# Performance work log

Measured on AMD Instinct MI355X. Metric: run time of the kernel, lower is better.

Reference implementation:

```python
import jax, jax.numpy as jnp
import numpy as np


def ternarize_weight(w):
    # abs-mean threshold quantization to {-am, 0, +am}
    abs_mean = jnp.maximum(jnp.abs(w).mean(), 1e-5)
    thr = 0.7 * abs_mean
    q = jnp.where(w > thr, 1.0, jnp.where(w < -thr, -1.0, 0.0))
    # STE: forward value is q*abs_mean, grad flows to w as identity
    return w + jax.lax.stop_gradient(q * abs_mean - w)


def rotate_half(x):
    x1, x2 = jnp.split(x, 2, axis=-1)
    return jnp.concatenate([-x2, x1], axis=-1)


def setup_inputs() -> dict:
    key = jax.random.key(0)
    k1, k2, k3, k4, k5 = jax.random.split(key, 5)
    B, T, C, H = 2, 2048, 1024, 16
    D = C // H
    x = jax.random.normal(k1, (B, T, C), dtype=jnp.float32)
    cos = jax.random.uniform(k2, (1, 1, T, D), dtype=jnp.float32)
    sin = jax.random.uniform(k3, (1, 1, T, D), dtype=jnp.float32)
    w_qkv = jax.random.normal(k4, (3 * C, C), dtype=jnp.float32) / np.sqrt(C)
    w_proj = jax.random.normal(k5, (C, C), dtype=jnp.float32) / np.sqrt(C)
    return {"x": x, "cos": cos, "sin": sin, "w_qkv": w_qkv, "w_proj": w_proj}


def reference(x, cos, sin, w_qkv, w_proj):
    B, T, C = x.shape
    H = 16
    D = C // H
    wq = ternarize_weight(w_qkv)
    wp = ternarize_weight(w_proj)
    qkv = x @ wq.T  # [B,T,3C]
    q, k, v = jnp.split(qkv, 3, axis=-1)
    # [B,T,C] -> [B,H,T,D]
    q = q.reshape(B, T, H, D).transpose(0, 2, 1, 3)
    k = k.reshape(B, T, H, D).transpose(0, 2, 1, 3)
    v = v.reshape(B, T, H, D).transpose(0, 2, 1, 3)
    # RoPE
    q = q * cos + rotate_half(q) * sin
    k = k * cos + rotate_half(k) * sin
    # causal SDPA
    scale = 1.0 / np.sqrt(D)
    scores = jnp.einsum("bhqd,bhkd->bhqk", q, k) * scale
    causal = jnp.tril(jnp.ones((T, T), dtype=bool))
    scores = jnp.where(causal, scores, jnp.finfo(scores.dtype).min)
    attn = jax.nn.softmax(scores, axis=-1)
    y = jnp.einsum("bhqk,bhkd->bhqd", attn, v)  # [B,H,T,D]
    y = y.transpose(0, 2, 1, 3).reshape(B, T, C)
    return y @ wp.T
```

## Files before the change

kernel.cpp:

```cpp
#include <hip/hip_runtime.h>
#include <hip/hip_bf16.h>

#define B_ 2
#define T_ 2048
#define C_ 1024
#define H_ 16
#define D_ 64
#define M_ 4096
#define N3C 3072

using short8  = __attribute__((ext_vector_type(8))) short;
using floatx4 = __attribute__((ext_vector_type(4))) float;
typedef unsigned int u32;

__device__ __forceinline__ unsigned short f2b(float f) {
  __hip_bfloat16 h = __float2bfloat16(f);
  return *reinterpret_cast<unsigned short*>(&h);
}
__device__ __forceinline__ float b2f(unsigned short u) {
  union { unsigned int i; float f; } x; x.i = ((unsigned int)u) << 16; return x.f;
}
__device__ __forceinline__ u32 pk2(float a, float b) {
  float2 t; t.x = a; t.y = b;
  __hip_bfloat162 p = __float22bfloat162_rn(t);
  return *reinterpret_cast<u32*>(&p);
}

__device__ __forceinline__ void gll16(const void* g, void* l) {
  __builtin_amdgcn_global_load_lds((const __attribute__((address_space(1))) u32*)g,
                                   (__attribute__((address_space(3))) u32*)l, 16, 0, 0);
}


__global__ void abs_sum2(const float* __restrict__ wq, const float* __restrict__ wp,
                         double* __restrict__ sums) {
  __shared__ double red[4];
  const float* w = blockIdx.y ? wp : wq;
  const int n4 = blockIdx.y ? (C_ * C_ / 4) : (3 * C_ * C_ / 4);
  int stride = gridDim.x * blockDim.x;
  double s = 0.0;
  for (int i = blockIdx.x * blockDim.x + threadIdx.x; i < n4; i += stride) {
    float4 v = ((const float4*)w)[i];
    s += (double)fabsf(v.x) + (double)fabsf(v.y) + (double)fabsf(v.z) + (double)fabsf(v.w);
  }
  #pragma unroll
  for (int off = 32; off > 0; off >>= 1)
    s += __shfl_down(s, off, 64);
  if ((threadIdx.x & 63) == 0) red[threadIdx.x >> 6] = s;
  __syncthreads();
  if (threadIdx.x == 0) atomicAdd(sums + blockIdx.y, (red[0] + red[1]) + (red[2] + red[3]));
}

__global__ void tern_cvt(const float* __restrict__ wq, const float* __restrict__ wp,
                         const float* __restrict__ x,
                         unsigned short* __restrict__ oq, unsigned short* __restrict__ op,
                         unsigned short* __restrict__ xb,
                         const double* __restrict__ sums, float* __restrict__ ams) {
  const int NQ = 3 * C_ * C_;
  const int NP = C_ * C_;
  int i = blockIdx.x * blockDim.x + threadIdx.x;
  float am0 = fmaxf((float)(sums[0] * (1.0 / NQ)), 1e-5f);
  float am1 = fmaxf((float)(sums[1] * (1.0 / NP)), 1e-5f);
  if (i == 0) { ams[0] = am0; ams[1] = am1; }
  if (i < NQ) {
    float thr = 0.7f * am0, v = wq[i];
    oq[i] = (v > thr) ? 0x3F80u : ((v < -thr) ? 0xBF80u : 0u);
  } else if (i < NQ + NP) {
    int j = i - NQ;
    float thr = 0.7f * am1, v = wp[j];
    op[j] = (v > thr) ? 0x3F80u : ((v < -thr) ? 0xBF80u : 0u);
  } else {
    int j = i - NQ - NP;
    float4 v = ((const float4*)x)[j];
    ushort4 o; o.x = f2b(v.x); o.y = f2b(v.y); o.z = f2b(v.z); o.w = f2b(v.w);
    ((ushort4*)xb)[j] = o;
  }
}


__global__ __launch_bounds__(256) void gemm_qkv(const unsigned short* __restrict__ A,
                                                const unsigned short* __restrict__ W,
                                                const float* __restrict__ scale_ptr,
                                                const float* __restrict__ cosp,
                                                const float* __restrict__ sinp,
                                                unsigned short* __restrict__ Qb,
                                                unsigned short* __restrict__ Kb,
                                                unsigned short* __restrict__ Vtb) {
  const int K = C_;
  __shared__ __attribute__((aligned(16))) unsigned short As[128 * 32];
  __shared__ __attribute__((aligned(16))) unsigned short Ws[128 * 32];
  const int tid = threadIdx.x, lane = tid & 63, wv = tid >> 6;
  const int m = lane & 15, g = lane >> 4;
  const int m0 = blockIdx.y * 128, n0 = blockIdx.x * 128;
  const int wm = (wv >> 1) * 64, wn = (wv & 1) * 64;

  const int srow = wv * 16 + (lane >> 2);
  const int skoff = (lane & 3) * 8;
  const unsigned short* ga0 = A + (size_t)(m0 + srow) * K + skoff;
  const unsigned short* ga1 = A + (size_t)(m0 + 64 + srow) * K + skoff;
  const unsigned short* gw0 = W + (size_t)(n0 + srow) * K + skoff;
  const unsigned short* gw1 = W + (size_t)(n0 + 64 + srow) * K + skoff;
  unsigned short* la0 = As + (wv * 16) * 32;
  unsigned short* la1 = As + (64 + wv * 16) * 32;
  unsigned short* lw0 = Ws + (wv * 16) * 32;
  unsigned short* lw1 = Ws + (64 + wv * 16) * 32;

  floatx4 acc[4][4] = {};
  for (int kc = 0; kc < K; kc += 32) {
    __syncthreads();
    gll16(ga0, la0); gll16(ga1, la1); gll16(gw0, lw0); gll16(gw1, lw1);
    ga0 += 32; ga1 += 32; gw0 += 32; gw1 += 32;
    __syncthreads();
    short8 af[4], wf[4];
    #pragma unroll
    for (int r = 0; r < 4; r++)
      af[r] = *(const short8*)&As[(wm + r * 16 + m) * 32 + g * 8];
    #pragma unroll
    for (int c = 0; c < 4; c++)
      wf[c] = *(const short8*)&Ws[(wn + c * 16 + m) * 32 + g * 8];
    #pragma unroll
    for (int r = 0; r < 4; r++)
      #pragma unroll
      for (int c = 0; c < 4; c++)
        acc[r][c] = __builtin_amdgcn_mfma_f32_16x16x32_bf16(af[r], wf[c], acc[r][c], 0, 0, 0);
  }

  const float am = *scale_ptr;
  const int sect = n0 >> 10;
  const int nloc = n0 & 1023;
  const int h = (nloc + wn) >> 6;
  if (sect < 2) {
    unsigned short* dst = sect ? Kb : Qb;
    const float sc = sect ? am : am * 0.18033688011112042f;
    #pragma unroll
    for (int r = 0; r < 4; r++)
      #pragma unroll
      for (int i = 0; i < 4; i++) {
        int row = m0 + wm + r * 16 + g * 4 + i;
        int t = row & (T_ - 1), b = row >> 11;
        size_t obase = ((size_t)(b * H_ + h) * T_ + t) * 64;
        #pragma unroll
        for (int c = 0; c < 4; c++) {
          int p = c * 16 + m;
          float cv = cosp[t * 64 + p], sv = sinp[t * 64 + p];
          float a = acc[r][c][i], pt = acc[r][c ^ 2][i];
          float val = (c < 2) ? (a * cv - pt * sv) : (a * cv + pt * sv);
          dst[obase + p] = f2b(val * sc);
        }
      }
  } else {
    #pragma unroll
    for (int r = 0; r < 4; r++)
      #pragma unroll
      for (int i = 0; i < 4; i++) {
        int row = m0 + wm + r * 16 + g * 4 + i;
        int t = row & (T_ - 1), b = row >> 11;
        size_t hbase = (size_t)(b * H_ + h) * 64 * T_;
        #pragma unroll
        for (int c = 0; c < 4; c++)
          Vtb[hbase + (size_t)(c * 16 + m) * T_ + t] = f2b(acc[r][c][i] * am);
      }
  }
}


__global__ __launch_bounds__(256) void gemm_proj(const unsigned short* __restrict__ A,
                                                 const unsigned short* __restrict__ W,
                                                 const float* __restrict__ scale_ptr,
                                                 float* __restrict__ Cout) {
  const int K = C_, N = C_;
  __shared__ __attribute__((aligned(16))) unsigned short As[128 * 32];
  __shared__ __attribute__((aligned(16))) unsigned short Ws[64 * 32];
  const int tid = threadIdx.x, lane = tid & 63, wv = tid >> 6;
  const int m = lane & 15, g = lane >> 4;
  const int m0 = blockIdx.y * 128, n0 = blockIdx.x * 64;
  const int wm = (wv >> 1) * 64, wn = (wv & 1) * 32;

  const int srow = wv * 16 + (lane >> 2);
  const int skoff = (lane & 3) * 8;
  const unsigned short* ga0 = A + (size_t)(m0 + srow) * K + skoff;
  const unsigned short* ga1 = A + (size_t)(m0 + 64 + srow) * K + skoff;
  const unsigned short* gw0 = W + (size_t)(n0 + srow) * K + skoff;
  unsigned short* la0 = As + (wv * 16) * 32;
  unsigned short* la1 = As + (64 + wv * 16) * 32;
  unsigned short* lw0 = Ws + (wv * 16) * 32;

  floatx4 acc[4][2] = {};
  for (int kc = 0; kc < K; kc += 32) {
    __syncthreads();
    gll16(ga0, la0); gll16(ga1, la1); gll16(gw0, lw0);
    ga0 += 32; ga1 += 32; gw0 += 32;
    __syncthreads();
    short8 af[4], wf[2];
    #pragma unroll
    for (int r = 0; r < 4; r++)
      af[r] = *(const short8*)&As[(wm + r * 16 + m) * 32 + g * 8];
    #pragma unroll
    for (int c = 0; c < 2; c++)
      wf[c] = *(const short8*)&Ws[(wn + c * 16 + m) * 32 + g * 8];
    #pragma unroll
    for (int r = 0; r < 4; r++)
      #pragma unroll
      for (int c = 0; c < 2; c++)
        acc[r][c] = __builtin_amdgcn_mfma_f32_16x16x32_bf16(af[r], wf[c], acc[r][c], 0, 0, 0);
  }

  const float scale = *scale_ptr;
  #pragma unroll
  for (int r = 0; r < 4; r++)
    #pragma unroll
    for (int c = 0; c < 2; c++)
      #pragma unroll
      for (int i = 0; i < 4; i++) {
        int row = m0 + wm + r * 16 + g * 4 + i;
        int col = n0 + wn + c * 16 + m;
        Cout[(size_t)row * N + col] = acc[r][c][i] * scale;
      }
}


__global__ __launch_bounds__(256) void flash_mfma(const unsigned short* __restrict__ Qb,
                                                  const unsigned short* __restrict__ Kb,
                                                  const unsigned short* __restrict__ Vtb,
                                                  unsigned short* __restrict__ Y) {
  __shared__ __align__(16) unsigned short Ktile[2][64][64];
  __shared__ __align__(16) unsigned short Vtile[2][64][64];
  __shared__ __align__(16) unsigned short Plds[4][16][72];
  const int lane = threadIdx.x & 63;
  const int wv = threadIdx.x >> 6;
  const int m = lane & 15, g = lane >> 4;
  const int gid = blockIdx.x;
  const int xcd = gid & 7, j = gid >> 3;
  const int bh = xcd * 4 + (j & 3);
  const int s = 31 - (j >> 2);
  const int b = bh >> 4, h = bh & 15;
  const size_t hb = (size_t)bh * T_ * 64;
  const unsigned short* Kbh = Kb + hb;
  const unsigned short* Vbh = Vtb + hb;
  const int r8 = lane >> 3, cc8 = lane & 7;
  const int gcol = ((cc8 ^ r8) << 3);

  const int ntiles = s + 1;
  const int qbase = s * 64 + wv * 16;
  const int q_glob = qbase + m;

  const unsigned short* qp = Qb + hb + (size_t)(qbase + m) * 64 + g * 8;
  short8 qf0 = *(const short8*)qp;
  short8 qf1 = *(const short8*)(qp + 32);

  short8 ones;
  #pragma unroll
  for (int i = 0; i < 8; i++) ones[i] = (short)0x3F80;

  floatx4 O[4] = {};
  floatx4 accl = {};

  #pragma unroll
  for (int cc = 0; cc < 2; cc++) {
    int row = wv * 16 + cc * 8;
    gll16(Kbh + (size_t)(row + r8) * 64 + gcol, &Ktile[0][row][0]);
    gll16(Vbh + (size_t)(row + r8) * T_ + gcol, &Vtile[0][row][0]);
  }

  for (int kt = 0; kt < ntiles; kt++) {
    const int buf = kt & 1;
    const int kb = kt * 64;
    __syncthreads();
    if (kt + 1 < ntiles) {
      const int kb2 = kb + 64;
      #pragma unroll
      for (int cc = 0; cc < 2; cc++) {
        int row = wv * 16 + cc * 8;
        gll16(Kbh + (size_t)(kb2 + row + r8) * 64 + gcol, &Ktile[1 - buf][row][0]);
        gll16(Vbh + (size_t)(row + r8) * T_ + kb2 + gcol, &Vtile[1 - buf][row][0]);
      }
    }
    floatx4 S[4];
    #pragma unroll
    for (int mt = 0; mt < 4; mt++) {
      int row = mt * 16 + m;
      short8 kf0 = *(const short8*)&Ktile[buf][row][(g ^ (m & 7)) << 3];
      short8 kf1 = *(const short8*)&Ktile[buf][row][((g + 4) ^ (m & 7)) << 3];
      floatx4 sv = {};
      sv = __builtin_amdgcn_mfma_f32_16x16x32_bf16(kf0, qf0, sv, 0, 0, 0);
      sv = __builtin_amdgcn_mfma_f32_16x16x32_bf16(kf1, qf1, sv, 0, 0, 0);
      S[mt] = sv;
    }
    if (kt + 1 < ntiles) {
      #pragma unroll
      for (int mt = 0; mt < 4; mt++) {
        uint2 w;
        w.x = pk2(exp2f(S[mt][0]), exp2f(S[mt][1]));
        w.y = pk2(exp2f(S[mt][2]), exp2f(S[mt][3]));
        *(uint2*)&Plds[wv][m][mt * 16 + g * 4] = w;
      }
    } else {
      #pragma unroll
      for (int mt = 0; mt < 4; mt++) {
        float e[4];
        #pragma unroll
        for (int r = 0; r < 4; r++) {
          int kg = kb + mt * 16 + g * 4 + r;
          e[r] = (kg <= q_glob) ? exp2f(S[mt][r]) : 0.f;
        }
        uint2 w;
        w.x = pk2(e[0], e[1]);
        w.y = pk2(e[2], e[3]);
        *(uint2*)&Plds[wv][m][mt * 16 + g * 4] = w;
      }
    }
    short8 pa0 = *(const short8*)&Plds[wv][m][g * 8];
    short8 pa1 = *(const short8*)&Plds[wv][m][32 + g * 8];
    #pragma unroll
    for (int nt = 0; nt < 4; nt++) {
      int row = nt * 16 + m;
      short8 v0 = *(const short8*)&Vtile[buf][row][(g ^ (m & 7)) << 3];
      short8 v1 = *(const short8*)&Vtile[buf][row][((g + 4) ^ (m & 7)) << 3];
      O[nt] = __builtin_amdgcn_mfma_f32_16x16x32_bf16(pa0, v0, O[nt], 0, 0, 0);
      O[nt] = __builtin_amdgcn_mfma_f32_16x16x32_bf16(pa1, v1, O[nt], 0, 0, 0);
    }
    accl = __builtin_amdgcn_mfma_f32_16x16x32_bf16(pa0, ones, accl, 0, 0, 0);
    accl = __builtin_amdgcn_mfma_f32_16x16x32_bf16(pa1, ones, accl, 0, 0, 0);
  }

  float li[4];
  #pragma unroll
  for (int r = 0; r < 4; r++) li[r] = 1.0f / accl[r];
  #pragma unroll
  for (int nt = 0; nt < 4; nt++)
    #pragma unroll
    for (int r = 0; r < 4; r++) {
      int trow = qbase + g * 4 + r;
      int col = h * 64 + nt * 16 + m;
      Y[(size_t)(b * T_ + trow) * C_ + col] = f2b(O[nt][r] * li[r]);
    }
}


extern "C" void kernel_launch(void* const* d_in, const int* in_sizes, int n_in,
                              void* d_out, int out_size, void* d_ws, size_t ws_size,
                              hipStream_t stream) {
  (void)in_sizes; (void)n_in; (void)out_size; (void)ws_size;
  const float* x      = (const float*)d_in[0];
  const float* cosp   = (const float*)d_in[1];
  const float* sinp   = (const float*)d_in[2];
  const float* w_qkv  = (const float*)d_in[3];
  const float* w_proj = (const float*)d_in[4];
  float* out = (float*)d_out;

  char* ws = (char*)d_ws;
  double* sums = (double*)ws;
  float*  ams  = (float*)(ws + 16);
  unsigned short* wqkv_b  = (unsigned short*)(ws + 256);
  unsigned short* wproj_b = wqkv_b + (size_t)N3C * C_;
  unsigned short* xb      = wproj_b + (size_t)C_ * C_;
  unsigned short* Qb      = xb + (size_t)M_ * C_;
  unsigned short* Kb      = Qb + (size_t)B_ * H_ * T_ * D_;
  unsigned short* Vtb     = Kb + (size_t)B_ * H_ * T_ * D_;
  unsigned short* yb      = Vtb + (size_t)B_ * H_ * T_ * D_;

  hipMemsetAsync(sums, 0, 16, stream);
  abs_sum2<<<dim3(256, 2), 256, 0, stream>>>(w_qkv, w_proj, sums);
  tern_cvt<<<(4 * C_ * C_ + M_ * C_ / 4) / 256, 256, 0, stream>>>(w_qkv, w_proj, x,
                                                                  wqkv_b, wproj_b, xb,
                                                                  sums, ams);
  gemm_qkv<<<dim3(N3C / 128, M_ / 128), 256, 0, stream>>>(xb, wqkv_b, ams + 0,
                                                          cosp, sinp, Qb, Kb, Vtb);
  flash_mfma<<<1024, 256, 0, stream>>>(Qb, Kb, Vtb, yb);
  gemm_proj<<<dim3(C_ / 64, M_ / 128), 256, 0, stream>>>(yb, wproj_b, ams + 1, out);
}
```

Measured before the change: 207.3 us.

## Double-buffer LDS tiles and XOR-swizzle layout in QKV and proj GEMMs

```diff
diff --git a/kernel.cpp b/kernel.cpp
--- a/kernel.cpp
+++ b/kernel.cpp
@@ -87,37 +87,43 @@
                                                 unsigned short* __restrict__ Kb,
                                                 unsigned short* __restrict__ Vtb) {
   const int K = C_;
-  __shared__ __attribute__((aligned(16))) unsigned short As[128 * 32];
-  __shared__ __attribute__((aligned(16))) unsigned short Ws[128 * 32];
+  __shared__ __attribute__((aligned(16))) unsigned short As[2][128 * 32];
+  __shared__ __attribute__((aligned(16))) unsigned short Ws[2][128 * 32];
   const int tid = threadIdx.x, lane = tid & 63, wv = tid >> 6;
   const int m = lane & 15, g = lane >> 4;
   const int m0 = blockIdx.y * 128, n0 = blockIdx.x * 128;
   const int wm = (wv >> 1) * 64, wn = (wv & 1) * 64;
 
   const int srow = wv * 16 + (lane >> 2);
-  const int skoff = (lane & 3) * 8;
+  const int skoff = (((lane & 3) ^ ((lane >> 2) & 3)) * 8);
   const unsigned short* ga0 = A + (size_t)(m0 + srow) * K + skoff;
   const unsigned short* ga1 = A + (size_t)(m0 + 64 + srow) * K + skoff;
   const unsigned short* gw0 = W + (size_t)(n0 + srow) * K + skoff;
   const unsigned short* gw1 = W + (size_t)(n0 + 64 + srow) * K + skoff;
-  unsigned short* la0 = As + (wv * 16) * 32;
-  unsigned short* la1 = As + (64 + wv * 16) * 32;
-  unsigned short* lw0 = Ws + (wv * 16) * 32;
-  unsigned short* lw1 = Ws + (64 + wv * 16) * 32;
+  const int oA0 = (wv * 16) * 32;
+  const int oA1 = (64 + wv * 16) * 32;
 
   floatx4 acc[4][4] = {};
+  gll16(ga0, &As[0][oA0]); gll16(ga1, &As[0][oA1]);
+  gll16(gw0, &Ws[0][oA0]); gll16(gw1, &Ws[0][oA1]);
+  ga0 += 32; ga1 += 32; gw0 += 32; gw1 += 32;
+
+  const int swz = (g ^ (m & 3)) << 3;
   for (int kc = 0; kc < K; kc += 32) {
+    const int buf = (kc >> 5) & 1;
     __syncthreads();
-    gll16(ga0, la0); gll16(ga1, la1); gll16(gw0, lw0); gll16(gw1, lw1);
-    ga0 += 32; ga1 += 32; gw0 += 32; gw1 += 32;
-    __syncthreads();
+    if (kc + 32 < K) {
+      gll16(ga0, &As[buf ^ 1][oA0]); gll16(ga1, &As[buf ^ 1][oA1]);
+      gll16(gw0, &Ws[buf ^ 1][oA0]); gll16(gw1, &Ws[buf ^ 1][oA1]);
+      ga0 += 32; ga1 += 32; gw0 += 32; gw1 += 32;
+    }
     short8 af[4], wf[4];
     #pragma unroll
     for (int r = 0; r < 4; r++)
-      af[r] = *(const short8*)&As[(wm + r * 16 + m) * 32 + g * 8];
+      af[r] = *(const short8*)&As[buf][(wm + r * 16 + m) * 32 + swz];
     #pragma unroll
     for (int c = 0; c < 4; c++)
-      wf[c] = *(const short8*)&Ws[(wn + c * 16 + m) * 32 + g * 8];
+      wf[c] = *(const short8*)&Ws[buf][(wn + c * 16 + m) * 32 + swz];
     #pragma unroll
     for (int r = 0; r < 4; r++)
       #pragma unroll
@@ -169,35 +175,41 @@
                                                  const float* __restrict__ scale_ptr,
                                                  float* __restrict__ Cout) {
   const int K = C_, N = C_;
-  __shared__ __attribute__((aligned(16))) unsigned short As[128 * 32];
-  __shared__ __attribute__((aligned(16))) unsigned short Ws[64 * 32];
+  __shared__ __attribute__((aligned(16))) unsigned short As[2][128 * 32];
+  __shared__ __attribute__((aligned(16))) unsigned short Ws[2][64 * 32];
   const int tid = threadIdx.x, lane = tid & 63, wv = tid >> 6;
   const int m = lane & 15, g = lane >> 4;
   const int m0 = blockIdx.y * 128, n0 = blockIdx.x * 64;
   const int wm = (wv >> 1) * 64, wn = (wv & 1) * 32;
 
   const int srow = wv * 16 + (lane >> 2);
-  const int skoff = (lane & 3) * 8;
+  const int skoff = (((lane & 3) ^ ((lane >> 2) & 3)) * 8);
   const unsigned short* ga0 = A + (size_t)(m0 + srow) * K + skoff;
   const unsigned short* ga1 = A + (size_t)(m0 + 64 + srow) * K + skoff;
   const unsigned short* gw0 = W + (size_t)(n0 + srow) * K + skoff;
-  unsigned short* la0 = As + (wv * 16) * 32;
-  unsigned short* la1 = As + (64 + wv * 16) * 32;
-  unsigned short* lw0 = Ws + (wv * 16) * 32;
+  const int oA0 = (wv * 16) * 32;
+  const int oA1 = (64 + wv * 16) * 32;
 
   floatx4 acc[4][2] = {};
+  gll16(ga0, &As[0][oA0]); gll16(ga1, &As[0][oA1]); gll16(gw0, &Ws[0][oA0]);
+  ga0 += 32; ga1 += 32; gw0 += 32;
+
+  const int swz = (g ^ (m & 3)) << 3;
   for (int kc = 0; kc < K; kc += 32) {
+    const int buf = (kc >> 5) & 1;
     __syncthreads();
-    gll16(ga0, la0); gll16(ga1, la1); gll16(gw0, lw0);
-    ga0 += 32; ga1 += 32; gw0 += 32;
-    __syncthreads();
+    if (kc + 32 < K) {
+      gll16(ga0, &As[buf ^ 1][oA0]); gll16(ga1, &As[buf ^ 1][oA1]);
+      gll16(gw0, &Ws[buf ^ 1][oA0]);
+      ga0 += 32; ga1 += 32; gw0 += 32;
+    }
     short8 af[4], wf[2];
     #pragma unroll
     for (int r = 0; r < 4; r++)
-      af[r] = *(const short8*)&As[(wm + r * 16 + m) * 32 + g * 8];
+      af[r] = *(const short8*)&As[buf][(wm + r * 16 + m) * 32 + swz];
     #pragma unroll
     for (int c = 0; c < 2; c++)
-      wf[c] = *(const short8*)&Ws[(wn + c * 16 + m) * 32 + g * 8];
+      wf[c] = *(const short8*)&Ws[buf][(wn + c * 16 + m) * 32 + swz];
     #pragma unroll
     for (int r = 0; r < 4; r++)
       #pragma unroll
```

New measurement: 213.9 us. 3.2% more time.

## Triple-buffer LDS staging in QKV and projection GEMMs with vmcnt-based sync

Applied to the files above, without the earlier changes.

```diff
diff --git a/kernel.cpp b/kernel.cpp
--- a/kernel.cpp
+++ b/kernel.cpp
@@ -30,6 +30,12 @@
   __builtin_amdgcn_global_load_lds((const __attribute__((address_space(1))) u32*)g,
                                    (__attribute__((address_space(3))) u32*)l, 16, 0, 0);
 }
+
+#define SYNCV(N) do {                                                   \
+    asm volatile("s_waitcnt vmcnt(" #N ")" ::: "memory");               \
+    __builtin_amdgcn_s_barrier();                                       \
+    asm volatile("" ::: "memory");                                      \
+  } while (0)
 
 
 __global__ void abs_sum2(const float* __restrict__ wq, const float* __restrict__ wp,
@@ -87,8 +93,8 @@
                                                 unsigned short* __restrict__ Kb,
                                                 unsigned short* __restrict__ Vtb) {
   const int K = C_;
-  __shared__ __attribute__((aligned(16))) unsigned short As[128 * 32];
-  __shared__ __attribute__((aligned(16))) unsigned short Ws[128 * 32];
+  __shared__ __attribute__((aligned(16))) unsigned short As[3][128 * 32];
+  __shared__ __attribute__((aligned(16))) unsigned short Ws[3][128 * 32];
   const int tid = threadIdx.x, lane = tid & 63, wv = tid >> 6;
   const int m = lane & 15, g = lane >> 4;
   const int m0 = blockIdx.y * 128, n0 = blockIdx.x * 128;
@@ -100,30 +106,44 @@
   const unsigned short* ga1 = A + (size_t)(m0 + 64 + srow) * K + skoff;
   const unsigned short* gw0 = W + (size_t)(n0 + srow) * K + skoff;
   const unsigned short* gw1 = W + (size_t)(n0 + 64 + srow) * K + skoff;
-  unsigned short* la0 = As + (wv * 16) * 32;
-  unsigned short* la1 = As + (64 + wv * 16) * 32;
-  unsigned short* lw0 = Ws + (wv * 16) * 32;
-  unsigned short* lw1 = Ws + (64 + wv * 16) * 32;
+  const int oA0 = (wv * 16) * 32;
+  const int oA1 = (64 + wv * 16) * 32;
 
   floatx4 acc[4][4] = {};
-  for (int kc = 0; kc < K; kc += 32) {
-    __syncthreads();
-    gll16(ga0, la0); gll16(ga1, la1); gll16(gw0, lw0); gll16(gw1, lw1);
-    ga0 += 32; ga1 += 32; gw0 += 32; gw1 += 32;
-    __syncthreads();
-    short8 af[4], wf[4];
-    #pragma unroll
-    for (int r = 0; r < 4; r++)
-      af[r] = *(const short8*)&As[(wm + r * 16 + m) * 32 + g * 8];
-    #pragma unroll
-    for (int c = 0; c < 4; c++)
-      wf[c] = *(const short8*)&Ws[(wn + c * 16 + m) * 32 + g * 8];
-    #pragma unroll
-    for (int r = 0; r < 4; r++)
-      #pragma unroll
-      for (int c = 0; c < 4; c++)
-        acc[r][c] = __builtin_amdgcn_mfma_f32_16x16x32_bf16(af[r], wf[c], acc[r][c], 0, 0, 0);
-  }
+
+#define QSTAGE(TGT) do {                                                  \
+    gll16(ga0, &As[TGT][oA0]); gll16(ga1, &As[TGT][oA1]);                 \
+    gll16(gw0, &Ws[TGT][oA0]); gll16(gw1, &Ws[TGT][oA1]);                 \
+    ga0 += 32; ga1 += 32; gw0 += 32; gw1 += 32;                           \
+  } while (0)
+
+#define QCOMP(CUR) do {                                                   \
+    short8 af[4], wf[4];                                                  \
+    _Pragma("unroll")                                                     \
+    for (int r = 0; r < 4; r++)                                           \
+      af[r] = *(const short8*)&As[CUR][(wm + r * 16 + m) * 32 + g * 8];   \
+    _Pragma("unroll")                                                     \
+    for (int c = 0; c < 4; c++)                                           \
+      wf[c] = *(const short8*)&Ws[CUR][(wn + c * 16 + m) * 32 + g * 8];   \
+    _Pragma("unroll")                                                     \
+    for (int r = 0; r < 4; r++)                                           \
+      _Pragma("unroll")                                                   \
+      for (int c = 0; c < 4; c++)                                         \
+        acc[r][c] = __builtin_amdgcn_mfma_f32_16x16x32_bf16(af[r], wf[c], acc[r][c], 0, 0, 0); \
+  } while (0)
+
+  QSTAGE(0);
+  QSTAGE(1);
+  SYNCV(4);
+  for (int tt = 0; tt < 10; ++tt) {
+    QSTAGE(2); QCOMP(0); SYNCV(4);
+    QSTAGE(0); QCOMP(1); SYNCV(4);
+    QSTAGE(1); QCOMP(2); SYNCV(4);
+  }
+  QCOMP(0); SYNCV(0);
+  QCOMP(1);
+#undef QSTAGE
+#undef QCOMP
 
   const float am = *scale_ptr;
   const int sect = n0 >> 10;
@@ -169,8 +189,8 @@
                                                  const float* __restrict__ scale_ptr,
                                                  float* __restrict__ Cout) {
   const int K = C_, N = C_;
-  __shared__ __attribute__((aligned(16))) unsigned short As[128 * 32];
-  __shared__ __attribute__((aligned(16))) unsigned short Ws[64 * 32];
+  __shared__ __attribute__((aligned(16))) unsigned short As[3][128 * 32];
+  __shared__ __attribute__((aligned(16))) unsigned short Ws[3][64 * 32];
   const int tid = threadIdx.x, lane = tid & 63, wv = tid >> 6;
   const int m = lane & 15, g = lane >> 4;
   const int m0 = blockIdx.y * 128, n0 = blockIdx.x * 64;
@@ -181,29 +201,44 @@
   const unsigned short* ga0 = A + (size_t)(m0 + srow) * K + skoff;
   const unsigned short* ga1 = A + (size_t)(m0 + 64 + srow) * K + skoff;
   const unsigned short* gw0 = W + (size_t)(n0 + srow) * K + skoff;
-  unsigned short* la0 = As + (wv * 16) * 32;
-  unsigned short* la1 = As + (64 + wv * 16) * 32;
-  unsigned short* lw0 = Ws + (wv * 16) * 32;
+  const int oA0 = (wv * 16) * 32;
+  const int oA1 = (64 + wv * 16) * 32;
 
   floatx4 acc[4][2] = {};
-  for (int kc = 0; kc < K; kc += 32) {
-    __syncthreads();
-    gll16(ga0, la0); gll16(ga1, la1); gll16(gw0, lw0);
-    ga0 += 32; ga1 += 32; gw0 += 32;
-    __syncthreads();
-    short8 af[4], wf[2];
-    #pragma unroll
-    for (int r = 0; r < 4; r++)
-      af[r] = *(const short8*)&As[(wm + r * 16 + m) * 32 + g * 8];
-    #pragma unroll
-    for (int c = 0; c < 2; c++)
-      wf[c] = *(const short8*)&Ws[(wn + c * 16 + m) * 32 + g * 8];
-    #pragma unroll
-    for (int r = 0; r < 4; r++)
-      #pragma unroll
-      for (int c = 0; c < 2; c++)
-        acc[r][c] = __builtin_amdgcn_mfma_f32_16x16x32_bf16(af[r], wf[c], acc[r][c], 0, 0, 0);
-  }
+
+#define PSTAGE(TGT) do {                                                  \
+    gll16(ga0, &As[TGT][oA0]); gll16(ga1, &As[TGT][oA1]);                 \
+    gll16(gw0, &Ws[TGT][oA0]);                                            \
+    ga0 += 32; ga1 += 32; gw0 += 32;                                      \
+  } while (0)
+
+#define PCOMP(CUR) do {                                                   \
+    short8 af[4], wf[2];                                                  \
+    _Pragma("unroll")                                                     \
+    for (int r = 0; r < 4; r++)                                           \
+      af[r] = *(const short8*)&As[CUR][(wm + r * 16 + m) * 32 + g * 8];   \
+    _Pragma("unroll")                                                     \
+    for (int c = 0; c < 2; c++)                                           \
+      wf[c] = *(const short8*)&Ws[CUR][(wn + c * 16 + m) * 32 + g * 8];   \
+    _Pragma("unroll")                                                     \
+    for (int r = 0; r < 4; r++)                                           \
+      _Pragma("unroll")                                                   \
+      for (int c = 0; c < 2; c++)                                         \
+        acc[r][c] = __builtin_amdgcn_mfma_f32_16x16x32_bf16(af[r], wf[c], acc[r][c], 0, 0, 0); \
+  } while (0)
+
+  PSTAGE(0);
+  PSTAGE(1);
+  SYNCV(3);
+  for (int tt = 0; tt < 10; ++tt) {
+    PSTAGE(2); PCOMP(0); SYNCV(3);
+    PSTAGE(0); PCOMP(1); SYNCV(3);
+    PSTAGE(1); PCOMP(2); SYNCV(3);
+  }
+  PCOMP(0); SYNCV(0);
+  PCOMP(1);
+#undef PSTAGE
+#undef PCOMP
 
   const float scale = *scale_ptr;
   #pragma unroll
```

Measured after the change: 203.8 us. Within noise of the previous version (-1.7%).
